# Performance work log

Measured on AMD Instinct MI355X. Metric: run time of the kernel, lower is better.

Reference implementation:

```python
import jax, jax.numpy as jnp
import numpy as np

NOUT1, NOUT2, NBINS, NFEAT = 12, 15, 4000, 6

def setup_inputs() -> dict:
    key = jax.random.key(0)
    ks = jax.random.split(key, 7)
    x = jax.random.normal(ks[0], (64, NFEAT, 500), dtype=jnp.float32)
    # Linear params stored torch-style: W[out, in], b[out]
    W1 = jax.random.normal(ks[1], (NOUT1, NFEAT), dtype=jnp.float32) * (1.0 / np.sqrt(NFEAT))
    b1 = jax.random.normal(ks[2], (NOUT1,), dtype=jnp.float32) * 0.01
    W2 = jax.random.normal(ks[3], (NOUT2, NOUT1), dtype=jnp.float32) * (1.0 / np.sqrt(NOUT1))
    b2 = jax.random.normal(ks[4], (NOUT2,), dtype=jnp.float32) * 0.01
    W3 = jax.random.normal(ks[5], (NBINS, NOUT2), dtype=jnp.float32) * (1.0 / np.sqrt(NOUT2))
    b3 = jax.random.normal(ks[6], (NBINS,), dtype=jnp.float32) * 0.01
    return {"x": x, "W1": W1, "b1": b1, "W2": W2, "b2": b2, "W3": W3, "b3": b3}

def _leaky(h):
    return jnp.where(h >= 0, h, 0.01 * h)

def reference(x, W1, b1, W2, b2, W3, b3):
    nEvts = x.shape[0]
    t = x.reshape(nEvts, NFEAT, -1).transpose(0, 2, 1)      # (E, T, 6)
    h = _leaky(jnp.einsum('etf,of->eto', t, W1) + b1)        # (E, T, 12)
    h = _leaky(jnp.einsum('eti,oi->eto', h, W2) + b2)        # (E, T, 15)
    h = jnp.einsum('eti,oi->eto', h, W3) + b3                # (E, T, 4000)
    h = jax.nn.softplus(h)
    return jnp.sum(h, axis=1)                                # (E, 4000)
```

## Files before the change

### kernel.cpp

```cpp
#include <hip/hip_runtime.h>

#define NOUT1 12
#define NOUT2 15
#define NBINS 4000
#define NFEAT 6
#define NT    500
#define NTPAD 512
#define NEVT  64
#define LOG2E 1.4426950408889634f
#define LN2   0.6931471805599453f

typedef __attribute__((ext_vector_type(4))) _Float16 f16x4;
typedef __attribute__((ext_vector_type(4))) float f32x4;
typedef __attribute__((ext_vector_type(2))) float f32x2;

__device__ __forceinline__ float leaky(float s) {
    return s >= 0.0f ? s : 0.01f * s;
}

__device__ __forceinline__ void sp2_acc(f32x2 d, f32x2& acc) {
    f32x2 u;
    u.x = __builtin_amdgcn_exp2f(-__builtin_fabsf(d.x));
    u.y = __builtin_amdgcn_exp2f(-__builtin_fabsf(d.y));
    acc += __builtin_elementwise_max(d, (f32x2)0.0f);
    f32x2 q = __builtin_elementwise_fma(u, (f32x2)0.175167f, (f32x2)(-0.602758f));
    q = __builtin_elementwise_fma(u, q, (f32x2)1.428718f);
    acc = __builtin_elementwise_fma(u, q, acc);
}

__device__ __forceinline__ unsigned short f16bits(float v) {
    return __builtin_bit_cast(unsigned short, (_Float16)v);
}

__device__ __forceinline__ void h2_row_f16(
    const float* __restrict__ x, int e, int t,
    const float* __restrict__ W1, const float* __restrict__ b1,
    const float* __restrict__ W2, const float* __restrict__ b2,
    unsigned int packed[8])
{
    float f[NFEAT];
    #pragma unroll
    for (int i = 0; i < NFEAT; ++i)
        f[i] = x[e * NFEAT * NT + i * NT + t];

    float h1[NOUT1];
    #pragma unroll
    for (int o = 0; o < NOUT1; ++o) {
        float s = b1[o];
        #pragma unroll
        for (int i = 0; i < NFEAT; ++i)
            s = fmaf(f[i], W1[o * NFEAT + i], s);
        h1[o] = leaky(s);
    }

    unsigned short hf[16];
    #pragma unroll
    for (int o = 0; o < NOUT2; ++o) {
        float s = b2[o];
        #pragma unroll
        for (int i = 0; i < NOUT1; ++i)
            s = fmaf(h1[i], W2[o * NOUT1 + i], s);
        hf[o] = f16bits(leaky(s));
    }
    hf[15] = f16bits(1.0f);
    #pragma unroll
    for (int j = 0; j < 8; ++j)
        packed[j] = (unsigned int)hf[2*j] | ((unsigned int)hf[2*j+1] << 16);
}

__global__ __launch_bounds__(256) void h2_prep(
    const float* __restrict__ x,
    const float* __restrict__ W1, const float* __restrict__ b1,
    const float* __restrict__ W2, const float* __restrict__ b2,
    uint2* __restrict__ wsA)
{
    const int e = blockIdx.x;
    const int t = blockIdx.y * 256 + threadIdx.x;
    unsigned int packed[8];
    if (t < NT) {
        h2_row_f16(x, e, t, W1, b1, W2, b2, packed);
    } else {
        #pragma unroll
        for (int j = 0; j < 8; ++j) packed[j] = 0;
    }
    uint2* dst = wsA + (size_t)e * 2048 + (t >> 4) * 64 + (t & 15);
    dst[0]  = make_uint2(packed[0], packed[1]);
    dst[16] = make_uint2(packed[2], packed[3]);
    dst[32] = make_uint2(packed[4], packed[5]);
    dst[48] = make_uint2(packed[6], packed[7]);
}

__global__ __launch_bounds__(256) void w3_prep(
    const float* __restrict__ W3, const float* __restrict__ b3,
    uint2* __restrict__ wsB)
{
    const int bin = blockIdx.x * 256 + threadIdx.x;
    if (bin >= NBINS) return;
    unsigned short wf[16];
    #pragma unroll
    for (int k = 0; k < NOUT2; ++k)
        wf[k] = f16bits(W3[bin * NOUT2 + k] * LOG2E);
    wf[15] = f16bits(b3[bin] * LOG2E);
    uint2* dst = wsB + (size_t)bin * 4;
    #pragma unroll
    for (int g = 0; g < 4; ++g)
        dst[g] = make_uint2((unsigned int)wf[4*g] | ((unsigned int)wf[4*g+1] << 16),
                            (unsigned int)wf[4*g+2] | ((unsigned int)wf[4*g+3] << 16));
}

__device__ __forceinline__ void kde_phase2(
    const uint2* __restrict__ h2lds,
    f16x4 B1, float* __restrict__ out, int binbase, int e, int lane)
{
    const int col = lane & 15;
    const int kg  = lane >> 4;
    const int bin = binbase + col;

    const f32x4 zero4 = {0.0f, 0.0f, 0.0f, 0.0f};
    f32x2 acc01 = {0.0f, 0.0f}, acc23 = {0.0f, 0.0f};
    const uint2* ap = h2lds + kg * 16 + col;

    #define TILE_BODY(areg)                                                        \
        {                                                                          \
            f16x4 av = __builtin_bit_cast(f16x4, areg);                            \
            f32x4 c = __builtin_amdgcn_mfma_f32_16x16x16f16(av, B1, zero4, 0, 0, 0); \
            f32x2 p01 = {c[0], c[1]};                                              \
            f32x2 p23 = {c[2], c[3]};                                              \
            sp2_acc(p01, acc01);                                                   \
            sp2_acc(p23, acc23);                                                   \
        }

    uint2 A[4];
    A[0] = ap[0 * 64];
    A[1] = ap[1 * 64];
    A[2] = ap[2 * 64];
    A[3] = ap[3 * 64];

    #pragma unroll
    for (int g = 0; g < 31; ++g) {
        uint2 cur = A[g & 3];
        if (g + 4 < 32)
            A[g & 3] = ap[(g + 4) * 64];
        TILE_BODY(cur)
    }
    {
        f16x4 av = __builtin_bit_cast(f16x4, A[3]);
        f32x4 c = __builtin_amdgcn_mfma_f32_16x16x16f16(av, B1, zero4, 0, 0, 0);
        if (kg == 0) {
            f32x2 p01 = {c[0], c[1]};
            f32x2 p23 = {c[2], c[3]};
            sp2_acc(p01, acc01);
            sp2_acc(p23, acc23);
        }
    }
    #undef TILE_BODY

    f32x2 s2 = acc01 + acc23;
    float sum = s2.x + s2.y;
    sum += __shfl_xor(sum, 16);
    sum += __shfl_xor(sum, 32);
    if (lane < 16 && bin < NBINS)
        out[e * NBINS + bin] = sum * LN2;
}

__global__ __launch_bounds__(512, 8) void kde_main(
    const uint2* __restrict__ wsA, const uint2* __restrict__ wsB,
    float* __restrict__ out)
{
    __shared__ uint2 h2lds[2048];
    const int tid   = threadIdx.x;
    const int chunk = blockIdx.x;
    const int e     = blockIdx.y;

    {
        uint4* l4 = reinterpret_cast<uint4*>(h2lds);
        const uint4* g4 = reinterpret_cast<const uint4*>(wsA + (size_t)e * 2048);
        l4[tid]       = g4[tid];
        l4[tid + 512] = g4[tid + 512];
    }

    const int wid  = tid >> 6;
    const int lane = tid & 63;
    const int binbase = chunk * 128 + wid * 16;
    const int col = lane & 15;
    const int kg  = lane >> 4;
    const int binc = (binbase + col < NBINS) ? binbase + col : NBINS - 1;
    f16x4 B1 = __builtin_bit_cast(f16x4, wsB[(size_t)binc * 4 + kg]);

    __syncthreads();
    if (binbase >= NBINS) return;

    kde_phase2(h2lds, B1, out, binbase, e, lane);
}

__global__ __launch_bounds__(512, 2) void kde_fused(
    const float* __restrict__ x,
    const float* __restrict__ W1, const float* __restrict__ b1,
    const float* __restrict__ W2, const float* __restrict__ b2,
    const float* __restrict__ W3, const float* __restrict__ b3,
    float* __restrict__ out)
{
    __shared__ uint2 h2lds[2048];
    const int tid   = threadIdx.x;
    const int chunk = blockIdx.x;
    const int e     = blockIdx.y;

    {
        unsigned int packed[8];
        if (tid < NT) {
            h2_row_f16(x, e, tid, W1, b1, W2, b2, packed);
        } else {
            #pragma unroll
            for (int j = 0; j < 8; ++j) packed[j] = 0;
        }
        uint2* dst = &h2lds[(tid >> 4) * 64 + (tid & 15)];
        dst[0]  = make_uint2(packed[0], packed[1]);
        dst[16] = make_uint2(packed[2], packed[3]);
        dst[32] = make_uint2(packed[4], packed[5]);
        dst[48] = make_uint2(packed[6], packed[7]);
    }

    const int wid  = tid >> 6;
    const int lane = tid & 63;
    const int binbase = chunk * 128 + wid * 16;
    const int col = lane & 15;
    const int kg  = lane >> 4;
    const int binc = (binbase + col < NBINS) ? binbase + col : NBINS - 1;
    f16x4 B1;
    #pragma unroll
    for (int j = 0; j < 4; ++j) {
        const int kk = kg * 4 + j;
        float w = (kk < NOUT2) ? W3[binc * NOUT2 + kk] * LOG2E
                               : b3[binc] * LOG2E;
        B1[j] = (_Float16)w;
    }

    __syncthreads();
    if (binbase >= NBINS) return;

    kde_phase2(h2lds, B1, out, binbase, e, lane);
}

extern "C" void kernel_launch(void* const* d_in, const int* in_sizes, int n_in,
                              void* d_out, int out_size, void* d_ws, size_t ws_size,
                              hipStream_t stream) {
    const float* x  = (const float*)d_in[0];
    const float* W1 = (const float*)d_in[1];
    const float* b1 = (const float*)d_in[2];
    const float* W2 = (const float*)d_in[3];
    const float* b2 = (const float*)d_in[4];
    const float* W3 = (const float*)d_in[5];
    const float* b3 = (const float*)d_in[6];
    float* out = (float*)d_out;

    const size_t wsA_bytes = (size_t)NEVT * 2048 * sizeof(uint2);
    const size_t wsB_bytes = (size_t)NBINS * 4 * sizeof(uint2);
    if (ws_size >= wsA_bytes + wsB_bytes) {
        uint2* wsA = (uint2*)d_ws;
        uint2* wsB = (uint2*)((char*)d_ws + wsA_bytes);
        dim3 pgrid(NEVT, 2);
        h2_prep<<<pgrid, 256, 0, stream>>>(x, W1, b1, W2, b2, wsA);
        w3_prep<<<16, 256, 0, stream>>>(W3, b3, wsB);
        dim3 grid(32, NEVT);
        kde_main<<<grid, 512, 0, stream>>>(wsA, wsB, out);
    } else {
        dim3 grid(32, NEVT);
        kde_fused<<<grid, 512, 0, stream>>>(x, W1, b1, W2, b2, W3, b3, out);
    }
}
```

Measured before the change: 37.92 us.

## Drop prep kernels and always launch the single fused kernel

Removes the two preprocessing kernels and the workspace-based main kernel, so every call runs the fused kernel. That kernel recomputes the first two layers and the W3 fp16 conversion inside each block, and its launch bound rises from 2 to 8 blocks per multiprocessor. This drops two extra launches and the round-trip through workspace memory. The cost is redundant per-block recomputation: each event's hidden rows are rebuilt by all 32 chunk blocks, and the tighter occupancy bound may cap registers.

```diff
diff --git a/kernel.cpp b/kernel.cpp
--- a/kernel.cpp
+++ b/kernel.cpp
@@ -68,46 +68,6 @@
         packed[j] = (unsigned int)hf[2*j] | ((unsigned int)hf[2*j+1] << 16);
 }
 
-__global__ __launch_bounds__(256) void h2_prep(
-    const float* __restrict__ x,
-    const float* __restrict__ W1, const float* __restrict__ b1,
-    const float* __restrict__ W2, const float* __restrict__ b2,
-    uint2* __restrict__ wsA)
-{
-    const int e = blockIdx.x;
-    const int t = blockIdx.y * 256 + threadIdx.x;
-    unsigned int packed[8];
-    if (t < NT) {
-        h2_row_f16(x, e, t, W1, b1, W2, b2, packed);
-    } else {
-        #pragma unroll
-        for (int j = 0; j < 8; ++j) packed[j] = 0;
-    }
-    uint2* dst = wsA + (size_t)e * 2048 + (t >> 4) * 64 + (t & 15);
-    dst[0]  = make_uint2(packed[0], packed[1]);
-    dst[16] = make_uint2(packed[2], packed[3]);
-    dst[32] = make_uint2(packed[4], packed[5]);
-    dst[48] = make_uint2(packed[6], packed[7]);
-}
-
-__global__ __launch_bounds__(256) void w3_prep(
-    const float* __restrict__ W3, const float* __restrict__ b3,
-    uint2* __restrict__ wsB)
-{
-    const int bin = blockIdx.x * 256 + threadIdx.x;
-    if (bin >= NBINS) return;
-    unsigned short wf[16];
-    #pragma unroll
-    for (int k = 0; k < NOUT2; ++k)
-        wf[k] = f16bits(W3[bin * NOUT2 + k] * LOG2E);
-    wf[15] = f16bits(b3[bin] * LOG2E);
-    uint2* dst = wsB + (size_t)bin * 4;
-    #pragma unroll
-    for (int g = 0; g < 4; ++g)
-        dst[g] = make_uint2((unsigned int)wf[4*g] | ((unsigned int)wf[4*g+1] << 16),
-                            (unsigned int)wf[4*g+2] | ((unsigned int)wf[4*g+3] << 16));
-}
-
 __device__ __forceinline__ void kde_phase2(
     const uint2* __restrict__ h2lds,
     f16x4 B1, float* __restrict__ out, int binbase, int e, int lane)
@@ -163,37 +123,7 @@
         out[e * NBINS + bin] = sum * LN2;
 }
 
-__global__ __launch_bounds__(512, 8) void kde_main(
-    const uint2* __restrict__ wsA, const uint2* __restrict__ wsB,
-    float* __restrict__ out)
-{
-    __shared__ uint2 h2lds[2048];
-    const int tid   = threadIdx.x;
-    const int chunk = blockIdx.x;
-    const int e     = blockIdx.y;
-
-    {
-        uint4* l4 = reinterpret_cast<uint4*>(h2lds);
-        const uint4* g4 = reinterpret_cast<const uint4*>(wsA + (size_t)e * 2048);
-        l4[tid]       = g4[tid];
-        l4[tid + 512] = g4[tid + 512];
-    }
-
-    const int wid  = tid >> 6;
-    const int lane = tid & 63;
-    const int binbase = chunk * 128 + wid * 16;
-    const int col = lane & 15;
-    const int kg  = lane >> 4;
-    const int binc = (binbase + col < NBINS) ? binbase + col : NBINS - 1;
-    f16x4 B1 = __builtin_bit_cast(f16x4, wsB[(size_t)binc * 4 + kg]);
-
-    __syncthreads();
-    if (binbase >= NBINS) return;
-
-    kde_phase2(h2lds, B1, out, binbase, e, lane);
-}
-
-__global__ __launch_bounds__(512, 2) void kde_fused(
+__global__ __launch_bounds__(512, 8) void kde_fused(
     const float* __restrict__ x,
     const float* __restrict__ W1, const float* __restrict__ b1,
     const float* __restrict__ W2, const float* __restrict__ b2,
@@ -253,18 +183,6 @@
     const float* b3 = (const float*)d_in[6];
     float* out = (float*)d_out;
 
-    const size_t wsA_bytes = (size_t)NEVT * 2048 * sizeof(uint2);
-    const size_t wsB_bytes = (size_t)NBINS * 4 * sizeof(uint2);
-    if (ws_size >= wsA_bytes + wsB_bytes) {
-        uint2* wsA = (uint2*)d_ws;
-        uint2* wsB = (uint2*)((char*)d_ws + wsA_bytes);
-        dim3 pgrid(NEVT, 2);
-        h2_prep<<<pgrid, 256, 0, stream>>>(x, W1, b1, W2, b2, wsA);
-        w3_prep<<<16, 256, 0, stream>>>(W3, b3, wsB);
-        dim3 grid(32, NEVT);
-        kde_main<<<grid, 512, 0, stream>>>(wsA, wsB, out);
-    } else {
-        dim3 grid(32, NEVT);
-        kde_fused<<<grid, 512, 0, stream>>>(x, W1, b1, W2, b2, W3, b3, out);
-    }
+    dim3 grid(32, NEVT);
+    kde_fused<<<grid, 512, 0, stream>>>(x, W1, b1, W2, b2, W3, b3, out);
 }
```

Result: slower. 44.58 us (+17.6%).

## Process two bin tiles per wave and merge prep kernels into one launch

Applied to the files above, without the earlier changes.

Each wave now computes 32 bins with two MFMAs sharing every LDS-loaded A tile, halving LDS traffic per bin and halving the grid. The two preprocessing kernels are merged into one launch to cut launch overhead. This costs more registers and accumulators per wave, and fewer waves are available to hide latency.

```diff
diff --git a/kernel.cpp b/kernel.cpp
--- a/kernel.cpp
+++ b/kernel.cpp
@@ -68,66 +68,87 @@
         packed[j] = (unsigned int)hf[2*j] | ((unsigned int)hf[2*j+1] << 16);
 }
 
-__global__ __launch_bounds__(256) void h2_prep(
+__global__ __launch_bounds__(256) void prep(
     const float* __restrict__ x,
     const float* __restrict__ W1, const float* __restrict__ b1,
     const float* __restrict__ W2, const float* __restrict__ b2,
-    uint2* __restrict__ wsA)
-{
-    const int e = blockIdx.x;
-    const int t = blockIdx.y * 256 + threadIdx.x;
-    unsigned int packed[8];
-    if (t < NT) {
-        h2_row_f16(x, e, t, W1, b1, W2, b2, packed);
+    const float* __restrict__ W3, const float* __restrict__ b3,
+    uint2* __restrict__ wsA, uint2* __restrict__ wsB)
+{
+    const int b = blockIdx.x;
+    if (b < 2 * NEVT) {
+        const int e = b >> 1;
+        const int t = (b & 1) * 256 + threadIdx.x;
+        unsigned int packed[8];
+        if (t < NT) {
+            h2_row_f16(x, e, t, W1, b1, W2, b2, packed);
+        } else {
+            #pragma unroll
+            for (int j = 0; j < 8; ++j) packed[j] = 0;
+        }
+        uint2* dst = wsA + (size_t)e * 2048 + (t >> 4) * 64 + (t & 15);
+        dst[0]  = make_uint2(packed[0], packed[1]);
+        dst[16] = make_uint2(packed[2], packed[3]);
+        dst[32] = make_uint2(packed[4], packed[5]);
+        dst[48] = make_uint2(packed[6], packed[7]);
     } else {
-        #pragma unroll
-        for (int j = 0; j < 8; ++j) packed[j] = 0;
-    }
-    uint2* dst = wsA + (size_t)e * 2048 + (t >> 4) * 64 + (t & 15);
-    dst[0]  = make_uint2(packed[0], packed[1]);
-    dst[16] = make_uint2(packed[2], packed[3]);
-    dst[32] = make_uint2(packed[4], packed[5]);
-    dst[48] = make_uint2(packed[6], packed[7]);
-}
-
-__global__ __launch_bounds__(256) void w3_prep(
-    const float* __restrict__ W3, const float* __restrict__ b3,
-    uint2* __restrict__ wsB)
-{
-    const int bin = blockIdx.x * 256 + threadIdx.x;
-    if (bin >= NBINS) return;
-    unsigned short wf[16];
-    #pragma unroll
-    for (int k = 0; k < NOUT2; ++k)
-        wf[k] = f16bits(W3[bin * NOUT2 + k] * LOG2E);
-    wf[15] = f16bits(b3[bin] * LOG2E);
-    uint2* dst = wsB + (size_t)bin * 4;
-    #pragma unroll
-    for (int g = 0; g < 4; ++g)
-        dst[g] = make_uint2((unsigned int)wf[4*g] | ((unsigned int)wf[4*g+1] << 16),
-                            (unsigned int)wf[4*g+2] | ((unsigned int)wf[4*g+3] << 16));
-}
-
-__device__ __forceinline__ void kde_phase2(
-    const uint2* __restrict__ h2lds,
-    f16x4 B1, float* __restrict__ out, int binbase, int e, int lane)
-{
-    const int col = lane & 15;
-    const int kg  = lane >> 4;
-    const int bin = binbase + col;
+        const int bin = (b - 2 * NEVT) * 256 + threadIdx.x;
+        if (bin >= NBINS) return;
+        unsigned short wf[16];
+        #pragma unroll
+        for (int k = 0; k < NOUT2; ++k)
+            wf[k] = f16bits(W3[bin * NOUT2 + k] * LOG2E);
+        wf[15] = f16bits(b3[bin] * LOG2E);
+        uint2* dst = wsB + (size_t)bin * 4;
+        #pragma unroll
+        for (int g = 0; g < 4; ++g)
+            dst[g] = make_uint2((unsigned int)wf[4*g] | ((unsigned int)wf[4*g+1] << 16),
+                                (unsigned int)wf[4*g+2] | ((unsigned int)wf[4*g+3] << 16));
+    }
+}
+
+__global__ __launch_bounds__(512, 8) void kde_main(
+    const uint2* __restrict__ wsA, const uint2* __restrict__ wsB,
+    float* __restrict__ out)
+{
+    __shared__ uint2 h2lds[2048];
+    const int tid   = threadIdx.x;
+    const int chunk = blockIdx.x;
+    const int e     = blockIdx.y;
+
+    {
+        uint4* l4 = reinterpret_cast<uint4*>(h2lds);
+        const uint4* g4 = reinterpret_cast<const uint4*>(wsA + (size_t)e * 2048);
+        l4[tid]       = g4[tid];
+        l4[tid + 512] = g4[tid + 512];
+    }
+
+    const int wid  = tid >> 6;
+    const int lane = tid & 63;
+    const int col  = lane & 15;
+    const int kg   = lane >> 4;
+    const int binbase = chunk * 256 + wid * 32;
+    const int bi0 = binbase + col      < NBINS ? binbase + col      : NBINS - 1;
+    const int bi1 = binbase + col + 16 < NBINS ? binbase + col + 16 : NBINS - 1;
+    f16x4 Ba = __builtin_bit_cast(f16x4, wsB[(size_t)bi0 * 4 + kg]);
+    f16x4 Bb = __builtin_bit_cast(f16x4, wsB[(size_t)bi1 * 4 + kg]);
+
+    __syncthreads();
+    if (binbase >= NBINS) return;
 
     const f32x4 zero4 = {0.0f, 0.0f, 0.0f, 0.0f};
-    f32x2 acc01 = {0.0f, 0.0f}, acc23 = {0.0f, 0.0f};
+    f32x2 accA0 = {0.f,0.f}, accA1 = accA0, accB0 = accA0, accB1 = accA0;
     const uint2* ap = h2lds + kg * 16 + col;
 
-    #define TILE_BODY(areg)                                                        \
-        {                                                                          \
-            f16x4 av = __builtin_bit_cast(f16x4, areg);                            \
-            f32x4 c = __builtin_amdgcn_mfma_f32_16x16x16f16(av, B1, zero4, 0, 0, 0); \
-            f32x2 p01 = {c[0], c[1]};                                              \
-            f32x2 p23 = {c[2], c[3]};                                              \
-            sp2_acc(p01, acc01);                                                   \
-            sp2_acc(p23, acc23);                                                   \
+    #define TILE_BODY(areg)                                                          \
+        {                                                                            \
+            f16x4 av = __builtin_bit_cast(f16x4, areg);                              \
+            f32x4 ca = __builtin_amdgcn_mfma_f32_16x16x16f16(av, Ba, zero4, 0, 0, 0);\
+            f32x4 cb = __builtin_amdgcn_mfma_f32_16x16x16f16(av, Bb, zero4, 0, 0, 0);\
+            f32x2 pa0 = {ca[0], ca[1]}, pa1 = {ca[2], ca[3]};                        \
+            f32x2 pb0 = {cb[0], cb[1]}, pb1 = {cb[2], cb[3]};                        \
+            sp2_acc(pa0, accA0); sp2_acc(pa1, accA1);                                \
+            sp2_acc(pb0, accB0); sp2_acc(pb1, accB1);                                \
         }
 
     uint2 A[4];
@@ -145,52 +166,29 @@
     }
     {
         f16x4 av = __builtin_bit_cast(f16x4, A[3]);
-        f32x4 c = __builtin_amdgcn_mfma_f32_16x16x16f16(av, B1, zero4, 0, 0, 0);
+        f32x4 ca = __builtin_amdgcn_mfma_f32_16x16x16f16(av, Ba, zero4, 0, 0, 0);
+        f32x4 cb = __builtin_amdgcn_mfma_f32_16x16x16f16(av, Bb, zero4, 0, 0, 0);
         if (kg == 0) {
-            f32x2 p01 = {c[0], c[1]};
-            f32x2 p23 = {c[2], c[3]};
-            sp2_acc(p01, acc01);
-            sp2_acc(p23, acc23);
+            f32x2 pa0 = {ca[0], ca[1]}, pa1 = {ca[2], ca[3]};
+            f32x2 pb0 = {cb[0], cb[1]}, pb1 = {cb[2], cb[3]};
+            sp2_acc(pa0, accA0); sp2_acc(pa1, accA1);
+            sp2_acc(pb0, accB0); sp2_acc(pb1, accB1);
         }
     }
     #undef TILE_BODY
 
-    f32x2 s2 = acc01 + acc23;
-    float sum = s2.x + s2.y;
-    sum += __shfl_xor(sum, 16);
-    sum += __shfl_xor(sum, 32);
-    if (lane < 16 && bin < NBINS)
-        out[e * NBINS + bin] = sum * LN2;
-}
-
-__global__ __launch_bounds__(512, 8) void kde_main(
-    const uint2* __restrict__ wsA, const uint2* __restrict__ wsB,
-    float* __restrict__ out)
-{
-    __shared__ uint2 h2lds[2048];
-    const int tid   = threadIdx.x;
-    const int chunk = blockIdx.x;
-    const int e     = blockIdx.y;
-
-    {
-        uint4* l4 = reinterpret_cast<uint4*>(h2lds);
-        const uint4* g4 = reinterpret_cast<const uint4*>(wsA + (size_t)e * 2048);
-        l4[tid]       = g4[tid];
-        l4[tid + 512] = g4[tid + 512];
-    }
-
-    const int wid  = tid >> 6;
-    const int lane = tid & 63;
-    const int binbase = chunk * 128 + wid * 16;
-    const int col = lane & 15;
-    const int kg  = lane >> 4;
-    const int binc = (binbase + col < NBINS) ? binbase + col : NBINS - 1;
-    f16x4 B1 = __builtin_bit_cast(f16x4, wsB[(size_t)binc * 4 + kg]);
-
-    __syncthreads();
-    if (binbase >= NBINS) return;
-
-    kde_phase2(h2lds, B1, out, binbase, e, lane);
+    f32x2 sA2 = accA0 + accA1;
+    f32x2 sB2 = accB0 + accB1;
+    float sumA = sA2.x + sA2.y;
+    float sumB = sB2.x + sB2.y;
+    sumA += __shfl_xor(sumA, 16);
+    sumA += __shfl_xor(sumA, 32);
+    sumB += __shfl_xor(sumB, 16);
+    sumB += __shfl_xor(sumB, 32);
+    if (lane < 16) {
+        out[e * NBINS + binbase + col]      = sumA * LN2;
+        out[e * NBINS + binbase + col + 16] = sumB * LN2;
+    }
 }
 
 __global__ __launch_bounds__(512, 2) void kde_fused(
@@ -222,23 +220,50 @@
 
     const int wid  = tid >> 6;
     const int lane = tid & 63;
-    const int binbase = chunk * 128 + wid * 16;
-    const int col = lane & 15;
-    const int kg  = lane >> 4;
-    const int binc = (binbase + col < NBINS) ? binbase + col : NBINS - 1;
-    f16x4 B1;
+    const int col  = lane & 15;
+    const int kg   = lane >> 4;
+    const int binbase = chunk * 256 + wid * 32;
+    const int bi0 = binbase + col      < NBINS ? binbase + col      : NBINS - 1;
+    const int bi1 = binbase + col + 16 < NBINS ? binbase + col + 16 : NBINS - 1;
+    f16x4 Ba, Bb;
     #pragma unroll
     for (int j = 0; j < 4; ++j) {
         const int kk = kg * 4 + j;
-        float w = (kk < NOUT2) ? W3[binc * NOUT2 + kk] * LOG2E
-                               : b3[binc] * LOG2E;
-        B1[j] = (_Float16)w;
+        Ba[j] = (_Float16)((kk < NOUT2) ? W3[bi0 * NOUT2 + kk] * LOG2E : b3[bi0] * LOG2E);
+        Bb[j] = (_Float16)((kk < NOUT2) ? W3[bi1 * NOUT2 + kk] * LOG2E : b3[bi1] * LOG2E);
     }
 
     __syncthreads();
     if (binbase >= NBINS) return;
 
-    kde_phase2(h2lds, B1, out, binbase, e, lane);
+    const f32x4 zero4 = {0.0f, 0.0f, 0.0f, 0.0f};
+    f32x2 accA0 = {0.f,0.f}, accA1 = accA0, accB0 = accA0, accB1 = accA0;
+    const uint2* ap = h2lds + kg * 16 + col;
+
+    #pragma unroll
+    for (int g = 0; g < 32; ++g) {
+        f16x4 av = __builtin_bit_cast(f16x4, ap[g * 64]);
+        f32x4 ca = __builtin_amdgcn_mfma_f32_16x16x16f16(av, Ba, zero4, 0, 0, 0);
+        f32x4 cb = __builtin_amdgcn_mfma_f32_16x16x16f16(av, Bb, zero4, 0, 0, 0);
+        if (g == 31 && kg != 0) break;
+        f32x2 pa0 = {ca[0], ca[1]}, pa1 = {ca[2], ca[3]};
+        f32x2 pb0 = {cb[0], cb[1]}, pb1 = {cb[2], cb[3]};
+        sp2_acc(pa0, accA0); sp2_acc(pa1, accA1);
+        sp2_acc(pb0, accB0); sp2_acc(pb1, accB1);
+    }
+
+    f32x2 sA2 = accA0 + accA1;
+    f32x2 sB2 = accB0 + accB1;
+    float sumA = sA2.x + sA2.y;
+    float sumB = sB2.x + sB2.y;
+    sumA += __shfl_xor(sumA, 16);
+    sumA += __shfl_xor(sumA, 32);
+    sumB += __shfl_xor(sumB, 16);
+    sumB += __shfl_xor(sumB, 32);
+    if (lane < 16) {
+        out[e * NBINS + binbase + col]      = sumA * LN2;
+        out[e * NBINS + binbase + col + 16] = sumB * LN2;
+    }
 }
 
 extern "C" void kernel_launch(void* const* d_in, const int* in_sizes, int n_in,
@@ -258,13 +283,12 @@
     if (ws_size >= wsA_bytes + wsB_bytes) {
         uint2* wsA = (uint2*)d_ws;
         uint2* wsB = (uint2*)((char*)d_ws + wsA_bytes);
-        dim3 pgrid(NEVT, 2);
-        h2_prep<<<pgrid, 256, 0, stream>>>(x, W1, b1, W2, b2, wsA);
-        w3_prep<<<16, 256, 0, stream>>>(W3, b3, wsB);
-        dim3 grid(32, NEVT);
+        prep<<<2 * NEVT + (NBINS + 255) / 256, 256, 0, stream>>>(
+            x, W1, b1, W2, b2, W3, b3, wsA, wsB);
+        dim3 grid(16, NEVT);
         kde_main<<<grid, 512, 0, stream>>>(wsA, wsB, out);
     } else {
-        dim3 grid(32, NEVT);
+        dim3 grid(16, NEVT);
         kde_fused<<<grid, 512, 0, stream>>>(x, W1, b1, W2, b2, W3, b3, out);
     }
 }
```

New measurement: 36.29 us, median of 3. 4.3% less time.
